# Performance work log

Measured on AMD Instinct MI355X. Metric: run time of the kernel, lower is better.

## Reference

```python
import jax, jax.numpy as jnp
import numpy as np

EPS = 1e-06


def setup_inputs() -> dict:
    key = jax.random.key(0)
    k1, k2, k3 = jax.random.split(key, 3)
    B, N, E, Din, U = 8, 1024, 16384, 128, 128
    x = jax.random.normal(k1, (B, N, Din), dtype=jnp.float32)
    node_mask = jnp.ones((B, N), dtype=bool)
    edge_index = jax.random.randint(k2, (B, 2, E), 0, N).astype(jnp.int32)
    edge_mask = jnp.ones((B, E), dtype=bool)
    kernel = jax.random.normal(k3, (Din, U), dtype=jnp.float32) * (1.0 / np.sqrt(Din))
    bias = jnp.zeros((U,), dtype=jnp.float32)
    return {"x": x, "node_mask": node_mask, "edge_index": edge_index,
            "edge_mask": edge_mask, "kernel": kernel, "bias": bias}


def reference(x, node_mask, edge_index, edge_mask, kernel, bias):
    B, N, _ = x.shape
    dtype = x.dtype
    node_mask_f = node_mask.astype(dtype)          # [B, N]
    edge_mask_f = edge_mask.astype(dtype)          # [B, E]
    src = jnp.clip(edge_index[:, 0, :], 0, N - 1)  # [B, E]
    dst = jnp.clip(edge_index[:, 1, :], 0, N - 1)  # [B, E]
    # adjacency[b, n, m] = sum over edges e with dst=n, src=m of edge_mask
    # (identical to the one-hot einsum in the original, built by scatter-add)
    b_idx = jnp.broadcast_to(jnp.arange(B)[:, None], src.shape)
    adjacency = jnp.zeros((B, N, N), dtype=dtype).at[b_idx, dst, src].add(edge_mask_f)
    # masked self-loops
    adjacency = adjacency + node_mask_f[:, :, None] * jnp.eye(N, dtype=dtype)[None]
    degree = jnp.sum(adjacency, axis=-1)           # [B, N]
    inv_sqrt_deg = jax.lax.rsqrt(jnp.maximum(degree, EPS))
    norm_adj = adjacency * inv_sqrt_deg[:, :, None] * inv_sqrt_deg[:, None, :]
    support = jnp.matmul(x, kernel)                # [B, N, U]
    out = jnp.matmul(norm_adj, support) + bias     # [B, N, U]
    return out * node_mask_f[:, :, None]
```

## Files before the change

kernel.cpp:

```cpp
#include <hip/hip_runtime.h>

#define B_   8
#define N_   1024
#define E_   16384
#define DIN_ 128
#define U_   128
#define CAP_ 64

__global__ __launch_bounds__(256) void k_support(
    const float* __restrict__ x, const float* __restrict__ kern,
    float* __restrict__ support, int* __restrict__ counts) {
    const int tid = threadIdx.x;
    const int u = tid & 127;
    const int h = tid >> 7;
    const int row0 = blockIdx.x * 16;
    if (tid < 16) counts[blockIdx.x * 16 + tid] = 0;
    __shared__ float xs[16][DIN_];
    const float4* xsrc = (const float4*)(x + (size_t)row0 * DIN_);
    #pragma unroll
    for (int i = 0; i < 2; ++i)
        ((float4*)xs)[i * 256 + tid] = xsrc[i * 256 + tid];
    __syncthreads();
    float acc[8] = {0.f,0.f,0.f,0.f,0.f,0.f,0.f,0.f};
    #pragma unroll 4
    for (int d = 0; d < DIN_; ++d) {
        float k = kern[d * U_ + u];
        #pragma unroll
        for (int r = 0; r < 8; ++r) acc[r] = fmaf(xs[h*8+r][d], k, acc[r]);
    }
    #pragma unroll
    for (int r = 0; r < 8; ++r)
        support[(size_t)(row0 + h*8 + r) * U_ + u] = acc[r];
}

__global__ __launch_bounds__(256) void k_fill(
    const int* __restrict__ edge_index, const int* __restrict__ edge_mask,
    int* __restrict__ counts, unsigned short* __restrict__ bucket) {
    int i = blockIdx.x * blockDim.x + threadIdx.x;
    int b = i >> 14;
    int e = i & (E_ - 1);
    if (edge_mask[i] != 0) {
        const int* p = edge_index + (size_t)b * 2 * E_;
        int src = min(max(p[e], 0), N_ - 1);
        int dst = min(max(p[E_ + e], 0), N_ - 1);
        int bn = b * N_ + dst;
        int pos = atomicAdd(&counts[bn], 1);
        if (pos < CAP_) bucket[(size_t)bn * CAP_ + pos] = (unsigned short)src;
    }
}

__global__ __launch_bounds__(256) void k_agg(
    const float* __restrict__ support, const int* __restrict__ node_mask,
    const int* __restrict__ counts, const unsigned short* __restrict__ bucket,
    const float* __restrict__ bias, float* __restrict__ out) {
    const int bi  = blockIdx.x;
    const int swz = (bi & 7) * 512 + (bi >> 3);
    const int h   = threadIdx.x >> 7;
    const int u   = threadIdx.x & 127;
    const int bn  = swz * 2 + h;
    const int b   = bn >> 10;

    __shared__ int2 sp[2][CAP_];

    int nm = node_mask[bn];
    int cnt_true = counts[bn];
    int cnt = min(cnt_true, CAP_);
    float isd_n = rsqrtf(fmaxf((float)cnt_true + (nm ? 1.0f : 0.0f), 1e-6f));
    const unsigned short* bk = bucket + (size_t)bn * CAP_;

    if (u < cnt) {
        int m  = bk[u];
        int gm = b * N_ + m;
        float w = rsqrtf(fmaxf((float)counts[gm] + (node_mask[gm] ? 1.0f : 0.0f), 1e-6f));
        sp[h][u] = make_int2(gm, __float_as_int(w));
    }
    __syncthreads();

    float bs = bias[u];
    float acc = nm ? isd_n * support[(size_t)bn * U_ + u] : 0.f;
    #pragma unroll 4
    for (int t = 0; t < cnt; ++t) {
        int2 p = sp[h][t];
        acc = fmaf(__int_as_float(p.y), support[(size_t)p.x * U_ + u], acc);
    }
    out[(size_t)bn * U_ + u] = nm ? fmaf(isd_n, acc, bs) : 0.f;
}

extern "C" void kernel_launch(void* const* d_in, const int* in_sizes, int n_in,
                              void* d_out, int out_size, void* d_ws, size_t ws_size,
                              hipStream_t stream) {
    const float* x         = (const float*)d_in[0];
    const int*   node_mask = (const int*)d_in[1];
    const int*   edge_index= (const int*)d_in[2];
    const int*   edge_mask = (const int*)d_in[3];
    const float* kern      = (const float*)d_in[4];
    const float* bias      = (const float*)d_in[5];
    float*       out       = (float*)d_out;

    char* ws = (char*)d_ws;
    size_t off = 0;
    float*          support = (float*)(ws + off);          off += (size_t)B_ * N_ * U_ * sizeof(float);
    int*            counts  = (int*)(ws + off);            off += (size_t)B_ * N_ * sizeof(int);
    unsigned short* bucket  = (unsigned short*)(ws + off); off += (size_t)B_ * N_ * CAP_ * sizeof(unsigned short);

    k_support<<<B_ * N_ / 16, 256, 0, stream>>>(x, kern, support, counts);
    k_fill<<<B_ * E_ / 256, 256, 0, stream>>>(edge_index, edge_mask, counts, bucket);
    k_agg<<<B_ * N_ / 2, 256, 0, stream>>>(support, node_mask, counts, bucket, bias, out);
}
```

Baseline: 29.78 us.

## Fuse support GEMM with edge bucketing using shared-memory atomics; vectorize aggregation

Merges the support matmul and edge-fill kernels into one launch. The first B blocks bucket edges per batch using LDS atomic counters instead of global atomics, and the remaining blocks compute the support GEMM with 1024-thread blocks. Aggregation now handles four nodes per block with float2 loads. This removes one launch and the global atomic traffic, but each batch's 16K edges are serialized onto a single block, which may become the critical path.

```diff
diff --git a/kernel.cpp b/kernel.cpp
--- a/kernel.cpp
+++ b/kernel.cpp
@@ -7,45 +7,58 @@
 #define U_   128
 #define CAP_ 64
 
-__global__ __launch_bounds__(256) void k_support(
+__global__ __launch_bounds__(1024) void k_fused1(
     const float* __restrict__ x, const float* __restrict__ kern,
-    float* __restrict__ support, int* __restrict__ counts) {
+    const int* __restrict__ edge_index, const int* __restrict__ edge_mask,
+    float* __restrict__ support, int* __restrict__ counts,
+    unsigned short* __restrict__ bucket) {
+    __shared__ float xs[32][DIN_];
     const int tid = threadIdx.x;
-    const int u = tid & 127;
-    const int h = tid >> 7;
-    const int row0 = blockIdx.x * 16;
-    if (tid < 16) counts[blockIdx.x * 16 + tid] = 0;
-    __shared__ float xs[16][DIN_];
-    const float4* xsrc = (const float4*)(x + (size_t)row0 * DIN_);
-    #pragma unroll
-    for (int i = 0; i < 2; ++i)
-        ((float4*)xs)[i * 256 + tid] = xsrc[i * 256 + tid];
-    __syncthreads();
-    float acc[8] = {0.f,0.f,0.f,0.f,0.f,0.f,0.f,0.f};
-    #pragma unroll 4
-    for (int d = 0; d < DIN_; ++d) {
-        float k = kern[d * U_ + u];
+
+    if (blockIdx.x < B_) {
+        const int b = blockIdx.x;
+        int* lcnt = (int*)xs;
+        lcnt[tid] = 0;
+        __syncthreads();
+        const int4* srcp = (const int4*)(edge_index + (size_t)b * 2 * E_);
+        const int4* dstp = (const int4*)(edge_index + (size_t)b * 2 * E_ + E_);
+        const int4* emp  = (const int4*)(edge_mask  + (size_t)b * E_);
+        unsigned short* bk = bucket + (size_t)b * N_ * CAP_;
         #pragma unroll
-        for (int r = 0; r < 8; ++r) acc[r] = fmaf(xs[h*8+r][d], k, acc[r]);
-    }
-    #pragma unroll
-    for (int r = 0; r < 8; ++r)
-        support[(size_t)(row0 + h*8 + r) * U_ + u] = acc[r];
-}
-
-__global__ __launch_bounds__(256) void k_fill(
-    const int* __restrict__ edge_index, const int* __restrict__ edge_mask,
-    int* __restrict__ counts, unsigned short* __restrict__ bucket) {
-    int i = blockIdx.x * blockDim.x + threadIdx.x;
-    int b = i >> 14;
-    int e = i & (E_ - 1);
-    if (edge_mask[i] != 0) {
-        const int* p = edge_index + (size_t)b * 2 * E_;
-        int src = min(max(p[e], 0), N_ - 1);
-        int dst = min(max(p[E_ + e], 0), N_ - 1);
-        int bn = b * N_ + dst;
-        int pos = atomicAdd(&counts[bn], 1);
-        if (pos < CAP_) bucket[(size_t)bn * CAP_ + pos] = (unsigned short)src;
+        for (int i = 0; i < 4; ++i) {
+            int idx = i * 1024 + tid;
+            int4 s4 = srcp[idx], d4 = dstp[idx], m4 = emp[idx];
+            #pragma unroll
+            for (int j = 0; j < 4; ++j) {
+                int m = (j == 0) ? m4.x : (j == 1) ? m4.y : (j == 2) ? m4.z : m4.w;
+                if (m != 0) {
+                    int s = (j == 0) ? s4.x : (j == 1) ? s4.y : (j == 2) ? s4.z : s4.w;
+                    int d = (j == 0) ? d4.x : (j == 1) ? d4.y : (j == 2) ? d4.z : d4.w;
+                    s = min(max(s, 0), N_ - 1);
+                    d = min(max(d, 0), N_ - 1);
+                    int slot = atomicAdd(&lcnt[d], 1);
+                    if (slot < CAP_) bk[(size_t)d * CAP_ + slot] = (unsigned short)s;
+                }
+            }
+        }
+        __syncthreads();
+        counts[b * N_ + tid] = lcnt[tid];
+    } else {
+        const int row0 = (blockIdx.x - B_) * 32;
+        const int u = tid & 127;
+        const int h = tid >> 7;
+        ((float4*)xs)[tid] = ((const float4*)(x + (size_t)row0 * DIN_))[tid];
+        __syncthreads();
+        float acc[4] = {0.f, 0.f, 0.f, 0.f};
+        #pragma unroll 4
+        for (int d = 0; d < DIN_; ++d) {
+            float k = kern[d * U_ + u];
+            #pragma unroll
+            for (int r = 0; r < 4; ++r) acc[r] = fmaf(xs[h*4+r][d], k, acc[r]);
+        }
+        #pragma unroll
+        for (int r = 0; r < 4; ++r)
+            support[(size_t)(row0 + h*4 + r) * U_ + u] = acc[r];
     }
 }
 
@@ -53,14 +66,13 @@
     const float* __restrict__ support, const int* __restrict__ node_mask,
     const int* __restrict__ counts, const unsigned short* __restrict__ bucket,
     const float* __restrict__ bias, float* __restrict__ out) {
-    const int bi  = blockIdx.x;
-    const int swz = (bi & 7) * 512 + (bi >> 3);
-    const int h   = threadIdx.x >> 7;
-    const int u   = threadIdx.x & 127;
-    const int bn  = swz * 2 + h;
-    const int b   = bn >> 10;
+    const int bi = blockIdx.x;
+    const int h  = threadIdx.x >> 6;
+    const int u2 = threadIdx.x & 63;
+    const int bn = (bi & 7) * N_ + (bi >> 3) * 4 + h;
+    const int b  = bn >> 10;
 
-    __shared__ int2 sp[2][CAP_];
+    __shared__ int2 sp[4][CAP_];
 
     int nm = node_mask[bn];
     int cnt_true = counts[bn];
@@ -68,22 +80,35 @@
     float isd_n = rsqrtf(fmaxf((float)cnt_true + (nm ? 1.0f : 0.0f), 1e-6f));
     const unsigned short* bk = bucket + (size_t)bn * CAP_;
 
-    if (u < cnt) {
-        int m  = bk[u];
+    if (u2 < cnt) {
+        int m  = bk[u2];
         int gm = b * N_ + m;
         float w = rsqrtf(fmaxf((float)counts[gm] + (node_mask[gm] ? 1.0f : 0.0f), 1e-6f));
-        sp[h][u] = make_int2(gm, __float_as_int(w));
+        sp[h][u2] = make_int2(gm, __float_as_int(w));
     }
     __syncthreads();
 
-    float bs = bias[u];
-    float acc = nm ? isd_n * support[(size_t)bn * U_ + u] : 0.f;
+    const float2* supp2 = (const float2*)support;
+    float2 bs = ((const float2*)bias)[u2];
+    float2 acc;
+    if (nm) {
+        float2 s = supp2[(size_t)bn * 64 + u2];
+        acc = make_float2(isd_n * s.x, isd_n * s.y);
+    } else {
+        acc = make_float2(0.f, 0.f);
+    }
     #pragma unroll 4
     for (int t = 0; t < cnt; ++t) {
         int2 p = sp[h][t];
-        acc = fmaf(__int_as_float(p.y), support[(size_t)p.x * U_ + u], acc);
+        float w = __int_as_float(p.y);
+        float2 s = supp2[(size_t)p.x * 64 + u2];
+        acc.x = fmaf(w, s.x, acc.x);
+        acc.y = fmaf(w, s.y, acc.y);
     }
-    out[(size_t)bn * U_ + u] = nm ? fmaf(isd_n, acc, bs) : 0.f;
+    float2 o;
+    o.x = nm ? fmaf(isd_n, acc.x, bs.x) : 0.f;
+    o.y = nm ? fmaf(isd_n, acc.y, bs.y) : 0.f;
+    ((float2*)out)[(size_t)bn * 64 + u2] = o;
 }
 
 extern "C" void kernel_launch(void* const* d_in, const int* in_sizes, int n_in,
@@ -103,7 +128,7 @@
     int*            counts  = (int*)(ws + off);            off += (size_t)B_ * N_ * sizeof(int);
     unsigned short* bucket  = (unsigned short*)(ws + off); off += (size_t)B_ * N_ * CAP_ * sizeof(unsigned short);
 
-    k_support<<<B_ * N_ / 16, 256, 0, stream>>>(x, kern, support, counts);
-    k_fill<<<B_ * E_ / 256, 256, 0, stream>>>(edge_index, edge_mask, counts, bucket);
-    k_agg<<<B_ * N_ / 2, 256, 0, stream>>>(support, node_mask, counts, bucket, bias, out);
+    k_fused1<<<B_ + B_ * N_ / 32, 1024, 0, stream>>>(x, kern, edge_index, edge_mask,
+                                                     support, counts, bucket);
+    k_agg<<<B_ * N_ / 4, 256, 0, stream>>>(support, node_mask, counts, bucket, bias, out);
 }
```

After: 32.63 us. +9.6%, slower.
